# Optimization experiments

Hardware: AMD Instinct MI355X
Metric: run time of the kernel (lower is better)

The kernel has to match this reference:

```python
import jax, jax.numpy as jnp
import numpy as np

B, N = 16, 16          # batch, boxes per image
H, W = 640, 640        # image size
PH, PW = 300, 300      # learned patch size
MIN_AREA = 60.0
MAX_ANG = 20.0 * np.pi / 180.0


def setup_inputs() -> dict:
    key = jax.random.key(0)
    k1, k2, k3 = jax.random.split(key, 3)
    images = jax.random.uniform(k1, (B, H, W, 3), jnp.float32, -1.0, 1.0)
    patch = jax.random.uniform(k2, (PH, PW, 3), jnp.float32, -1.0, 1.0)
    kb1, kb2, kb3 = jax.random.split(k3, 3)
    ymin = jax.random.uniform(kb1, (B, N), jnp.float32, 0.0, H - 220.0)
    xmin = jax.random.uniform(kb2, (B, N), jnp.float32, 0.0, W - 220.0)
    hw = jax.random.uniform(kb3, (B, N, 2), jnp.float32, 100.0, 200.0)
    boxes = jnp.stack([ymin, xmin, ymin + hw[..., 0], xmin + hw[..., 1]], axis=-1)
    scale = jnp.float32(0.4)
    return {"boxes": boxes, "images": images, "patch": patch, "scale": scale}


def _bilinear(img, ys, xs):
    # img [Ph,Pw,3]; ys,xs [H,W] continuous source coords -> [H,W,3]
    Ph, Pw = img.shape[0], img.shape[1]
    y0 = jnp.floor(ys)
    x0 = jnp.floor(xs)
    wy = (ys - y0)[..., None]
    wx = (xs - x0)[..., None]
    y0i = jnp.clip(y0.astype(jnp.int32), 0, Ph - 1)
    y1i = jnp.clip(y0i + 1, 0, Ph - 1)
    x0i = jnp.clip(x0.astype(jnp.int32), 0, Pw - 1)
    x1i = jnp.clip(x0i + 1, 0, Pw - 1)
    v00 = img[y0i, x0i]
    v01 = img[y0i, x1i]
    v10 = img[y1i, x0i]
    v11 = img[y1i, x1i]
    return v00 * (1 - wy) * (1 - wx) + v01 * (1 - wy) * wx + v10 * wy * (1 - wx) + v11 * wy * wx


def _per_image(img, boxes_i, patch, scale, key):
    # random_print_adjust: per-channel affine jitter of the patch
    kw, kb, kloop = jax.random.split(key, 3)
    w = jax.random.normal(kw, (1, 1, 3), jnp.float32) * 0.1 + 0.5
    b = jax.random.normal(kb, (1, 1, 3), jnp.float32) * 0.01
    p = jnp.clip(w * patch + b, -1.0, 1.0)
    # BrightnessMatcher: shift patch mean brightness to match the image
    p = jnp.clip(p + (jnp.mean(img) - jnp.mean(p)), -1.0, 1.0)

    oimg = img
    mask0 = jnp.zeros_like(img)
    yy, xx = jnp.meshgrid(jnp.arange(H, dtype=jnp.float32),
                          jnp.arange(W, dtype=jnp.float32), indexing="ij")

    def step(carry, inp):
        image, mask = carry
        box, kk = inp
        ymin, xmin, ymax, xmax = box[0], box[1], box[2], box[3]
        h = ymax - ymin
        ww = xmax - xmin
        longer = jnp.maximum(h, ww)
        ps = jnp.floor(longer * scale)                       # patch_h == patch_w
        diag = jnp.minimum(jnp.sqrt(2.0).astype(jnp.float32) * ps, jnp.float32(W))
        oy = ymin + h / 2.0
        ox = xmin + ww / 2.0
        y0 = jnp.maximum(oy - diag / 2.0, 0.0)
        x0 = jnp.maximum(ox - diag / 2.0, 0.0)
        y0 = jnp.where(y0 + diag > H, H - diag, y0)
        x0 = jnp.where(x0 + diag > W, W - diag, x0)
        # int casts as in the TF code (values are >= 0, trunc == floor)
        y0i = jnp.floor(y0)
        x0i = jnp.floor(x0)
        phi = jnp.maximum(jnp.floor(ps), 1.0)
        diagi = jnp.floor(diag)
        valid_box = (phi * phi) > MIN_AREA

        k1, k2, k3 = jax.random.split(kk, 3)
        angle = jax.random.uniform(k1, (), jnp.float32, -MAX_ANG, MAX_ANG)

        # inverse warp: output pixel -> padded-patch coords -> resized-patch coords
        u = yy - y0i
        v = xx - x0i
        in_sq = (u >= 0) & (v >= 0) & (u < diagi) & (v < diagi)
        c = (diagi - 1.0) / 2.0
        ca, sa = jnp.cos(angle), jnp.sin(angle)
        su = c + ca * (u - c) - sa * (v - c)
        sv = c + sa * (u - c) + ca * (v - c)
        top = jnp.floor((diagi - phi) / 2.0)   # pad offset (floor top/left)
        py = su - top
        px = sv - top
        valid_src = (py >= 0) & (py <= phi - 1) & (px >= 0) & (px <= phi - 1)
        # resized-patch coords -> original patch coords (bilinear resize, half-pixel)
        sy = (py + 0.5) * (PH / phi) - 0.5
        sx = (px + 0.5) * (PW / phi) - 0.5
        samp = _bilinear(p, sy, sx)                                   # [H,W,3]
        noise = jax.random.uniform(k2, samp.shape, jnp.float32, -0.1, 0.1)
        bright = jax.random.uniform(k3, (), jnp.float32, -0.3, 0.3)
        im = jnp.clip(samp + noise + bright, -1.0, 1.0)
        val = jnp.where(valid_src[..., None], im, -2.0)
        val = jnp.where(val < -1.0, image, val)   # fill with current background
        val = jnp.clip(val, -1.0, 1.0)
        sel = (in_sq & valid_box)[..., None]
        new_image = jnp.where(sel, val, image)
        new_mask = jnp.where(sel, oimg - val, mask)
        return (new_image, new_mask), None

    keys = jax.random.split(kloop, N)
    (img_out, mask_out), _ = jax.lax.scan(step, (img, mask0), (boxes_i, keys))
    return img_out, mask_out


def reference(boxes, images, patch, scale):
    keys = jax.random.split(jax.random.key(42), B)
    img_out, mask_out = jax.vmap(_per_image, in_axes=(0, 0, None, None, 0))(
        images, boxes, patch, scale, keys)
    return img_out, mask_out
```

## Files before the change

### kernel.cpp

```cpp
#include <hip/hip_runtime.h>
#include <stdint.h>
#include <math.h>

#define B_ 16
#define N_ 16
#define H_ 640
#define W_ 640
#define PH_ 300
#define PW_ 300

#define IMG_ELEMS (H_*W_*3)
#define PATCH_ELEMS (PH_*PW_*3)

#define TROWS 16
#define TCOLS 64
#define TILES_Y (H_/TROWS)
#define TILES_X (W_/TCOLS)
#define TILES_PER_IMG (TILES_Y*TILES_X)
#define NTILES (B_*TILES_PER_IMG)
#define MAIN_GRID 2048

typedef float f32x4 __attribute__((ext_vector_type(4)));

__device__ __forceinline__ uint2 tf2x32(uint32_t k0, uint32_t k1, uint32_t x0, uint32_t x1) {
  uint32_t k2 = k0 ^ k1 ^ 0x1BD11BDAu;
#define TFR(r) x0 += x1; x1 = (x1 << (r)) | (x1 >> (32 - (r))); x1 ^= x0;
  x0 += k0; x1 += k1;
  TFR(13) TFR(15) TFR(26) TFR(6)
  x0 += k1; x1 += k2 + 1u;
  TFR(17) TFR(29) TFR(16) TFR(24)
  x0 += k2; x1 += k0 + 2u;
  TFR(13) TFR(15) TFR(26) TFR(6)
  x0 += k0; x1 += k1 + 3u;
  TFR(17) TFR(29) TFR(16) TFR(24)
  x0 += k1; x1 += k2 + 4u;
  TFR(13) TFR(15) TFR(26) TFR(6)
  x0 += k2; x1 += k0 + 5u;
#undef TFR
  return make_uint2(x0, x1);
}

__device__ __forceinline__ uint32_t rb32(uint32_t k0, uint32_t k1, uint32_t i) {
  uint2 o = tf2x32(k0, k1, 0u, i);
  return o.x ^ o.y;
}

__device__ __forceinline__ float u01f(uint32_t bits) {
  return __uint_as_float((bits >> 9) | 0x3F800000u) - 1.0f;
}

__device__ __forceinline__ float erfinv32(float x) {
  float w = -log1pf(-x * x);
  float p;
  if (w < 5.0f) {
    w = w - 2.5f;
    p = 2.81022636e-08f;
    p = fmaf(p, w, 3.43273939e-07f);
    p = fmaf(p, w, -3.5233877e-06f);
    p = fmaf(p, w, -4.39150654e-06f);
    p = fmaf(p, w, 0.00021858087f);
    p = fmaf(p, w, -0.00125372503f);
    p = fmaf(p, w, -0.00417768164f);
    p = fmaf(p, w, 0.246640727f);
    p = fmaf(p, w, 1.50140941f);
  } else {
    w = sqrtf(w) - 3.0f;
    p = -0.000200214257f;
    p = fmaf(p, w, 0.000100950558f);
    p = fmaf(p, w, 0.00134934322f);
    p = fmaf(p, w, -0.00367342844f);
    p = fmaf(p, w, 0.00573950773f);
    p = fmaf(p, w, -0.0076224613f);
    p = fmaf(p, w, 0.00943887047f);
    p = fmaf(p, w, 1.00167406f);
    p = fmaf(p, w, 2.83297682f);
  }
  return p * x;
}

__device__ __forceinline__ float jnormal(uint32_t bits) {
  float lo = __uint_as_float(0xBF7FFFFFu);
  float span = 1.0f - lo;
  float u = fmaxf(lo, u01f(bits) * span + lo);
  return 1.4142135623730951f * erfinv32(u);
}

__global__ __launch_bounds__(256) void reduce_kernel(
    const float* __restrict__ images, const float* __restrict__ patch,
    double* __restrict__ partials) {
  int b = blockIdx.y, j = blockIdx.x, t = threadIdx.x;
  __shared__ float swb[6];
  if (t < 6) {
    uint2 kb  = tf2x32(0u, 42u, 0u, (uint32_t)b);
    uint2 kw  = tf2x32(kb.x, kb.y, 0u, 0u);
    uint2 kbk = tf2x32(kb.x, kb.y, 0u, 1u);
    swb[t] = (t < 3) ? (jnormal(rb32(kw.x,  kw.y,  (uint32_t)t)) * 0.1f + 0.5f)
                     : (jnormal(rb32(kbk.x, kbk.y, (uint32_t)(t - 3))) * 0.01f);
  }
  __syncthreads();
  const float* img = images + (size_t)b * IMG_ELEMS;
  double s = 0.0;
  for (int i = j * 256 + t; i < IMG_ELEMS; i += 64 * 256) s += (double)img[i];
  float w0 = swb[0], w1 = swb[1], w2 = swb[2];
  float b0 = swb[3], b1 = swb[4], b2 = swb[5];
  double sp = 0.0;
  for (int i = j * 256 + t; i < PATCH_ELEMS; i += 64 * 256) {
    int q = i / 3; int ch = i - q * 3;
    float wv = (ch == 0) ? w0 : ((ch == 1) ? w1 : w2);
    float bv = (ch == 0) ? b0 : ((ch == 1) ? b1 : b2);
    float pv = fminf(fmaxf(wv * patch[i] + bv, -1.0f), 1.0f);
    sp += (double)pv;
  }
  __shared__ double sh[256];
  sh[t] = s; __syncthreads();
  for (int o = 128; o > 0; o >>= 1) { if (t < o) sh[t] += sh[t + o]; __syncthreads(); }
  if (t == 0) partials[((size_t)b * 64 + j) * 2 + 0] = sh[0];
  __syncthreads();
  sh[t] = sp; __syncthreads();
  for (int o = 128; o > 0; o >>= 1) { if (t < o) sh[t] += sh[t + o]; __syncthreads(); }
  if (t == 0) partials[((size_t)b * 64 + j) * 2 + 1] = sh[0];
}

__global__ void setup_finalize_kernel(
    const float* __restrict__ boxes, const float* __restrict__ scale_p,
    const double* __restrict__ partials,
    float* __restrict__ params, float* __restrict__ wb, float* __restrict__ dvals) {
  int t = threadIdx.x;
  if (t < B_) {
    double si = 0.0, sp = 0.0;
    for (int j = 0; j < 64; j++) {
      si += partials[((size_t)t * 64 + j) * 2 + 0];
      sp += partials[((size_t)t * 64 + j) * 2 + 1];
    }
    float mi = (float)(si / (double)IMG_ELEMS);
    float mp = (float)(sp / (double)PATCH_ELEMS);
    dvals[t] = mi - mp;
  }
  if (t >= B_*N_) return;
  int b = t >> 4, n = t & 15;
  uint2 kb = tf2x32(0u, 42u, 0u, (uint32_t)b);
  uint2 kw  = tf2x32(kb.x, kb.y, 0u, 0u);
  uint2 kbk = tf2x32(kb.x, kb.y, 0u, 1u);
  uint2 kl  = tf2x32(kb.x, kb.y, 0u, 2u);
  if (n == 0) {
    wb[b*8+0] = jnormal(rb32(kw.x,  kw.y,  0u)) * 0.1f + 0.5f;
    wb[b*8+1] = jnormal(rb32(kw.x,  kw.y,  1u)) * 0.1f + 0.5f;
    wb[b*8+2] = jnormal(rb32(kw.x,  kw.y,  2u)) * 0.1f + 0.5f;
    wb[b*8+3] = jnormal(rb32(kbk.x, kbk.y, 0u)) * 0.01f;
    wb[b*8+4] = jnormal(rb32(kbk.x, kbk.y, 1u)) * 0.01f;
    wb[b*8+5] = jnormal(rb32(kbk.x, kbk.y, 2u)) * 0.01f;
  }
  uint2 kk = tf2x32(kl.x, kl.y, 0u, (uint32_t)n);
  uint2 k1 = tf2x32(kk.x, kk.y, 0u, 0u);
  uint2 k2 = tf2x32(kk.x, kk.y, 0u, 1u);
  uint2 k3 = tf2x32(kk.x, kk.y, 0u, 2u);
  const float MA = (float)(20.0 * 3.14159265358979323846 / 180.0);
  float angle  = fmaxf(-MA,   u01f(rb32(k1.x, k1.y, 0u)) * (MA - (-MA)) + (-MA));
  float bright = fmaxf(-0.3f, u01f(rb32(k3.x, k3.y, 0u)) * (0.3f - (-0.3f)) + (-0.3f));

  const float* bx = boxes + (size_t)t * 4;
  float ymin = bx[0], xmin = bx[1], ymax = bx[2], xmax = bx[3];
  float sc = scale_p[0];
  float h = ymax - ymin, ww = xmax - xmin;
  float longer = fmaxf(h, ww);
  float ps = floorf(longer * sc);
  float diag = fminf(sqrtf(2.0f) * ps, (float)W_);
  float oy = ymin + h * 0.5f;
  float ox = xmin + ww * 0.5f;
  float y0 = fmaxf(oy - diag * 0.5f, 0.0f);
  float x0 = fmaxf(ox - diag * 0.5f, 0.0f);
  if (y0 + diag > (float)H_) y0 = (float)H_ - diag;
  if (x0 + diag > (float)W_) x0 = (float)W_ - diag;
  float y0i = floorf(y0), x0i = floorf(x0);
  float phi = fmaxf(floorf(ps), 1.0f);
  float diagi = floorf(diag);
  float validf = ((phi * phi) > 60.0f) ? 1.0f : 0.0f;
  float c = (diagi - 1.0f) * 0.5f;
  float top = floorf((diagi - phi) * 0.5f);

  float* P = params + t * 16;
  P[0] = y0i; P[1] = x0i; P[2] = diagi; P[3] = phi;
  P[4] = c;
  P[5] = (float)cos((double)angle);
  P[6] = (float)sin((double)angle);
  P[7] = top;
  P[8] = bright; P[9] = (float)PH_ / phi; P[10] = 0.0f; P[11] = validf;
  P[12] = __uint_as_float(k2.x); P[13] = __uint_as_float(k2.y); P[14] = 0.0f; P[15] = 0.0f;
}

__global__ __launch_bounds__(256) void main_kernel(
    const float* __restrict__ images, const float* __restrict__ patch,
    const float* __restrict__ params, const float* __restrict__ wb,
    const float* __restrict__ dvals, float* __restrict__ out) {
  __shared__ float sP[N_ * 16];
  __shared__ float sWB[6];
  __shared__ float sT[TROWS * 192];

  int bid = blockIdx.x;
  int b  = (bid & 7) * 2 + ((bid >> 3) & 1);
  int tid = threadIdx.x;

  if (tid < N_ * 16) sP[tid] = params[b * N_ * 16 + tid];
  if (tid < 6) sWB[tid] = wb[b * 8 + tid];
  __syncthreads();

  int lane = tid & 63;
  int wv   = tid >> 6;
  size_t ibase = (size_t)b * IMG_ELEMS;
  size_t moff  = (size_t)B_ * IMG_ELEMS;
  float dsh = dvals[b];

  int ck[3], lrk[3];
#pragma unroll
  for (int k = 0; k < 3; k++) {
    int t4 = k * 64 + lane;
    int r  = t4 / 48;
    ck[k]  = t4 - r * 48;
    lrk[k] = wv * 4 + r;
  }

  const float* Pc = sP + (tid & 15) * 16;
  float cP0 = Pc[0], cP1 = Pc[1], cLast = Pc[2] - 1.0f;
  bool cValid = (Pc[11] != 0.0f);

  for (int g = bid; g < NTILES; g += MAIN_GRID) {
    int tl = g >> 4;
    int ty = tl / TILES_X;
    int tx = tl - ty * TILES_X;

    float ys = (float)(ty * TROWS), ye = ys + (float)(TROWS - 1);
    float xs = (float)(tx * TCOLS), xe = xs + (float)(TCOLS - 1);
    bool hit = cValid && !(cP0 + cLast < ys || cP0 > ye)
                      && !(cP1 + cLast < xs || cP1 > xe);
    uint32_t mask = (uint32_t)(__ballot(hit) & 0xFFFFull);

    size_t fbk[3];
#pragma unroll
    for (int k = 0; k < 3; k++)
      fbk[k] = ibase + ((size_t)(ty * TROWS + lrk[k]) * W_ + tx * TCOLS) * 3 + (size_t)ck[k] * 4;

    if (mask == 0u) {
      const f32x4 z = {0.0f, 0.0f, 0.0f, 0.0f};
#pragma unroll
      for (int k = 0; k < 3; k++) {
        f32x4 d = *(const f32x4*)(images + fbk[k]);
        *(f32x4*)(out + fbk[k]) = d;
        *(f32x4*)(out + moff + fbk[k]) = z;
      }
      continue;
    }

#pragma unroll
    for (int k = 0; k < 3; k++) {
      f32x4 d = *(const f32x4*)(images + fbk[k]);
      *(f32x4*)(&sT[lrk[k] * 192 + ck[k] * 4]) = d;
    }

    int   pj[4];  float yfj[4];
    float xf = (float)(tx * TCOLS + lane);
#pragma unroll
    for (int j = 0; j < 4; j++) {
      int row = ty * TROWS + wv * 4 + j;
      pj[j]  = row * W_ + tx * TCOLS + lane;
      yfj[j] = (float)row;
    }

    float orig[12], img[12], mkv[12];
#pragma unroll
    for (int j = 0; j < 4; j++) {
      int base = (wv * 4 + j) * 192 + lane * 3;
      orig[j*3+0] = sT[base + 0];
      orig[j*3+1] = sT[base + 1];
      orig[j*3+2] = sT[base + 2];
    }
#pragma unroll
    for (int e = 0; e < 12; e++) { img[e] = orig[e]; mkv[e] = 0.0f; }

    uint32_t m = mask;
    while (m) {
      int n = __builtin_ctz(m);
      m &= m - 1u;
      const float* P = sP + n * 16;
      float P0 = P[0], P1 = P[1], diagi = P[2];
      float phi = P[3], c = P[4], ca = P[5], sa = P[6], top = P[7], bright = P[8], sph = P[9];
      uint32_t k2a = __float_as_uint(P[12]);
      uint32_t k2b = __float_as_uint(P[13]);
      float v = xf - P1;
      bool vok = (v >= 0.0f && v < diagi);
      float t2 = v - c;
#pragma unroll
      for (int j = 0; j < 4; j++) {
        float u = yfj[j] - P0;
        if (!(u >= 0.0f && u < diagi)) continue;
        if (!vok) continue;
        float t1 = u - c;
        float su = (c + ca * t1) - sa * t2;
        float sv = (c + sa * t1) + ca * t2;
        float py = su - top;
        float px = sv - top;
        bool vsrc = (py >= 0.0f) && (py <= phi - 1.0f) && (px >= 0.0f) && (px <= phi - 1.0f);
        if (vsrc) {
          float sy = (py + 0.5f) * sph - 0.5f;
          float sx = (px + 0.5f) * sph - 0.5f;
          float fy = floorf(sy), fx = floorf(sx);
          float wy = sy - fy, wxv = sx - fx;
          int iy0 = min(max((int)fy, 0), PH_ - 1);
          int iy1 = min(iy0 + 1, PH_ - 1);
          int ix0 = min(max((int)fx, 0), PW_ - 1);
          int ix1 = min(ix0 + 1, PW_ - 1);
          int o00 = (iy0 * PW_ + ix0) * 3;
          int o01 = (iy0 * PW_ + ix1) * 3;
          int o10 = (iy1 * PW_ + ix0) * 3;
          int o11 = (iy1 * PW_ + ix1) * 3;
          float omwy = 1.0f - wy, omwx = 1.0f - wxv;
          int nbase = pj[j] * 3;
#pragma unroll
          for (int ch = 0; ch < 3; ch++) {
            float wv2 = sWB[ch], bv = sWB[3 + ch];
            float a00 = fminf(fmaxf(wv2 * patch[o00 + ch] + bv, -1.0f), 1.0f);
            float a01 = fminf(fmaxf(wv2 * patch[o01 + ch] + bv, -1.0f), 1.0f);
            float a10 = fminf(fmaxf(wv2 * patch[o10 + ch] + bv, -1.0f), 1.0f);
            float a11 = fminf(fmaxf(wv2 * patch[o11 + ch] + bv, -1.0f), 1.0f);
            a00 = fminf(fmaxf(a00 + dsh, -1.0f), 1.0f);
            a01 = fminf(fmaxf(a01 + dsh, -1.0f), 1.0f);
            a10 = fminf(fmaxf(a10 + dsh, -1.0f), 1.0f);
            a11 = fminf(fmaxf(a11 + dsh, -1.0f), 1.0f);
            float samp = ((a00 * omwy) * omwx) + ((a01 * omwy) * wxv)
                       + ((a10 * wy) * omwx) + ((a11 * wy) * wxv);
            uint32_t bits = rb32(k2a, k2b, (uint32_t)(nbase + ch));
            float nz = fmaxf(-0.1f, u01f(bits) * (0.1f - (-0.1f)) + (-0.1f));
            float imv = fminf(fmaxf((samp + nz) + bright, -1.0f), 1.0f);
            img[j * 3 + ch] = imv;
            mkv[j * 3 + ch] = orig[j * 3 + ch] - imv;
          }
        } else {
#pragma unroll
          for (int ch = 0; ch < 3; ch++) mkv[j * 3 + ch] = orig[j * 3 + ch] - img[j * 3 + ch];
        }
      }
    }

#pragma unroll
    for (int j = 0; j < 4; j++) {
      int base = (wv * 4 + j) * 192 + lane * 3;
      sT[base + 0] = img[j*3+0];
      sT[base + 1] = img[j*3+1];
      sT[base + 2] = img[j*3+2];
    }
#pragma unroll
    for (int k = 0; k < 3; k++) {
      f32x4 d = *(const f32x4*)(&sT[lrk[k] * 192 + ck[k] * 4]);
      *(f32x4*)(out + fbk[k]) = d;
    }
#pragma unroll
    for (int j = 0; j < 4; j++) {
      int base = (wv * 4 + j) * 192 + lane * 3;
      sT[base + 0] = mkv[j*3+0];
      sT[base + 1] = mkv[j*3+1];
      sT[base + 2] = mkv[j*3+2];
    }
#pragma unroll
    for (int k = 0; k < 3; k++) {
      f32x4 d = *(const f32x4*)(&sT[lrk[k] * 192 + ck[k] * 4]);
      *(f32x4*)(out + moff + fbk[k]) = d;
    }
  }
}

extern "C" void kernel_launch(void* const* d_in, const int* in_sizes, int n_in,
                              void* d_out, int out_size, void* d_ws, size_t ws_size,
                              hipStream_t stream) {
  const float* boxes  = (const float*)d_in[0];
  const float* images = (const float*)d_in[1];
  const float* patch  = (const float*)d_in[2];
  const float* scale  = (const float*)d_in[3];
  float* out = (float*)d_out;

  float* params = (float*)d_ws;
  float* wb     = params + B_ * N_ * 16;
  float* dvals  = wb + B_ * 8;
  double* partials = (double*)((char*)d_ws + 20480);

  reduce_kernel<<<dim3(64, B_), 256, 0, stream>>>(images, patch, partials);
  setup_finalize_kernel<<<1, 256, 0, stream>>>(boxes, scale, partials, params, wb, dvals);
  main_kernel<<<MAIN_GRID, 256, 0, stream>>>(images, patch, params, wb, dvals, out);
}
```

Baseline: 291.3 us.

## Fuse reduce, setup and main kernels into one persistent kernel with grid barrier

Merges the mean-reduction, per-box parameter setup and main compositing kernels into a single persistent launch of 1024 blocks. Each block computes its own box parameters in shared memory and one slice of the reduction, then copies tiles no box touches while it waits on an atomic-counter grid barrier. After the barrier it reads all partial sums to get the brightness shift and composites the tiles that boxes hit. This removes two kernel launches and overlaps the reduction with the untouched-tile copy, but it adds a memset, a spin-wait barrier that deadlocks unless all 1024 blocks are resident at once, and a smaller grid.

New measurement: 434.6 us. +49.2%, slower.

```diff
diff --git a/kernel.cpp b/kernel.cpp
--- a/kernel.cpp
+++ b/kernel.cpp
@@ -18,7 +18,7 @@
 #define TILES_X (W_/TCOLS)
 #define TILES_PER_IMG (TILES_Y*TILES_X)
 #define NTILES (B_*TILES_PER_IMG)
-#define MAIN_GRID 2048
+#define GRID_N 1024
 
 typedef float f32x4 __attribute__((ext_vector_type(4)));
 
@@ -85,131 +85,111 @@
   return 1.4142135623730951f * erfinv32(u);
 }
 
-__global__ __launch_bounds__(256) void reduce_kernel(
+__global__ __launch_bounds__(256, 4) void fused_kernel(
+    const float* __restrict__ boxes, const float* __restrict__ scale_p,
     const float* __restrict__ images, const float* __restrict__ patch,
-    double* __restrict__ partials) {
-  int b = blockIdx.y, j = blockIdx.x, t = threadIdx.x;
-  __shared__ float swb[6];
-  if (t < 6) {
+    double* partials, unsigned int* cnt, float* __restrict__ out) {
+  __shared__ float sP[N_ * 16];
+  __shared__ float sWB[6];
+  __shared__ float swbR[6];
+  __shared__ float sD[1];
+  __shared__ double sh[256];
+  __shared__ float sT[TROWS * 192];
+
+  int bid = blockIdx.x;
+  int tid = threadIdx.x;
+  int b   = (bid & 7) * 2 + ((bid >> 3) & 1);
+  int jr  = bid & 63;
+  int br  = bid >> 6;
+
+  if (tid < N_) {
+    int n = tid;
+    int t = b * N_ + n;
+    uint2 kb = tf2x32(0u, 42u, 0u, (uint32_t)b);
+    uint2 kl = tf2x32(kb.x, kb.y, 0u, 2u);
+    uint2 kk = tf2x32(kl.x, kl.y, 0u, (uint32_t)n);
+    uint2 k1 = tf2x32(kk.x, kk.y, 0u, 0u);
+    uint2 k2 = tf2x32(kk.x, kk.y, 0u, 1u);
+    uint2 k3 = tf2x32(kk.x, kk.y, 0u, 2u);
+    const float MA = (float)(20.0 * 3.14159265358979323846 / 180.0);
+    float angle  = fmaxf(-MA,   u01f(rb32(k1.x, k1.y, 0u)) * (MA - (-MA)) + (-MA));
+    float bright = fmaxf(-0.3f, u01f(rb32(k3.x, k3.y, 0u)) * (0.3f - (-0.3f)) + (-0.3f));
+
+    const float* bx = boxes + (size_t)t * 4;
+    float ymin = bx[0], xmin = bx[1], ymax = bx[2], xmax = bx[3];
+    float sc = scale_p[0];
+    float h = ymax - ymin, ww = xmax - xmin;
+    float longer = fmaxf(h, ww);
+    float ps = floorf(longer * sc);
+    float diag = fminf(sqrtf(2.0f) * ps, (float)W_);
+    float oy = ymin + h * 0.5f;
+    float ox = xmin + ww * 0.5f;
+    float y0 = fmaxf(oy - diag * 0.5f, 0.0f);
+    float x0 = fmaxf(ox - diag * 0.5f, 0.0f);
+    if (y0 + diag > (float)H_) y0 = (float)H_ - diag;
+    if (x0 + diag > (float)W_) x0 = (float)W_ - diag;
+    float y0i = floorf(y0), x0i = floorf(x0);
+    float phi = fmaxf(floorf(ps), 1.0f);
+    float diagi = floorf(diag);
+    float validf = ((phi * phi) > 60.0f) ? 1.0f : 0.0f;
+    float c = (diagi - 1.0f) * 0.5f;
+    float top = floorf((diagi - phi) * 0.5f);
+
+    float* P = sP + n * 16;
+    P[0] = y0i; P[1] = x0i; P[2] = diagi; P[3] = phi;
+    P[4] = c;
+    P[5] = (float)cos((double)angle);
+    P[6] = (float)sin((double)angle);
+    P[7] = top;
+    P[8] = bright; P[9] = (float)PH_ / phi; P[10] = 0.0f; P[11] = validf;
+    P[12] = __uint_as_float(k2.x); P[13] = __uint_as_float(k2.y);
+    P[14] = 0.0f; P[15] = 0.0f;
+  }
+  if (tid < 6) {
     uint2 kb  = tf2x32(0u, 42u, 0u, (uint32_t)b);
     uint2 kw  = tf2x32(kb.x, kb.y, 0u, 0u);
     uint2 kbk = tf2x32(kb.x, kb.y, 0u, 1u);
-    swb[t] = (t < 3) ? (jnormal(rb32(kw.x,  kw.y,  (uint32_t)t)) * 0.1f + 0.5f)
-                     : (jnormal(rb32(kbk.x, kbk.y, (uint32_t)(t - 3))) * 0.01f);
+    sWB[tid] = (tid < 3) ? (jnormal(rb32(kw.x,  kw.y,  (uint32_t)tid)) * 0.1f + 0.5f)
+                         : (jnormal(rb32(kbk.x, kbk.y, (uint32_t)(tid - 3))) * 0.01f);
+    uint2 kbR  = tf2x32(0u, 42u, 0u, (uint32_t)br);
+    uint2 kwR  = tf2x32(kbR.x, kbR.y, 0u, 0u);
+    uint2 kbkR = tf2x32(kbR.x, kbR.y, 0u, 1u);
+    swbR[tid] = (tid < 3) ? (jnormal(rb32(kwR.x,  kwR.y,  (uint32_t)tid)) * 0.1f + 0.5f)
+                          : (jnormal(rb32(kbkR.x, kbkR.y, (uint32_t)(tid - 3))) * 0.01f);
   }
   __syncthreads();
-  const float* img = images + (size_t)b * IMG_ELEMS;
-  double s = 0.0;
-  for (int i = j * 256 + t; i < IMG_ELEMS; i += 64 * 256) s += (double)img[i];
-  float w0 = swb[0], w1 = swb[1], w2 = swb[2];
-  float b0 = swb[3], b1 = swb[4], b2 = swb[5];
-  double sp = 0.0;
-  for (int i = j * 256 + t; i < PATCH_ELEMS; i += 64 * 256) {
-    int q = i / 3; int ch = i - q * 3;
-    float wv = (ch == 0) ? w0 : ((ch == 1) ? w1 : w2);
-    float bv = (ch == 0) ? b0 : ((ch == 1) ? b1 : b2);
-    float pv = fminf(fmaxf(wv * patch[i] + bv, -1.0f), 1.0f);
-    sp += (double)pv;
-  }
-  __shared__ double sh[256];
-  sh[t] = s; __syncthreads();
-  for (int o = 128; o > 0; o >>= 1) { if (t < o) sh[t] += sh[t + o]; __syncthreads(); }
-  if (t == 0) partials[((size_t)b * 64 + j) * 2 + 0] = sh[0];
-  __syncthreads();
-  sh[t] = sp; __syncthreads();
-  for (int o = 128; o > 0; o >>= 1) { if (t < o) sh[t] += sh[t + o]; __syncthreads(); }
-  if (t == 0) partials[((size_t)b * 64 + j) * 2 + 1] = sh[0];
-}
-
-__global__ void setup_finalize_kernel(
-    const float* __restrict__ boxes, const float* __restrict__ scale_p,
-    const double* __restrict__ partials,
-    float* __restrict__ params, float* __restrict__ wb, float* __restrict__ dvals) {
-  int t = threadIdx.x;
-  if (t < B_) {
-    double si = 0.0, sp = 0.0;
-    for (int j = 0; j < 64; j++) {
-      si += partials[((size_t)t * 64 + j) * 2 + 0];
-      sp += partials[((size_t)t * 64 + j) * 2 + 1];
-    }
-    float mi = (float)(si / (double)IMG_ELEMS);
-    float mp = (float)(sp / (double)PATCH_ELEMS);
-    dvals[t] = mi - mp;
-  }
-  if (t >= B_*N_) return;
-  int b = t >> 4, n = t & 15;
-  uint2 kb = tf2x32(0u, 42u, 0u, (uint32_t)b);
-  uint2 kw  = tf2x32(kb.x, kb.y, 0u, 0u);
-  uint2 kbk = tf2x32(kb.x, kb.y, 0u, 1u);
-  uint2 kl  = tf2x32(kb.x, kb.y, 0u, 2u);
-  if (n == 0) {
-    wb[b*8+0] = jnormal(rb32(kw.x,  kw.y,  0u)) * 0.1f + 0.5f;
-    wb[b*8+1] = jnormal(rb32(kw.x,  kw.y,  1u)) * 0.1f + 0.5f;
-    wb[b*8+2] = jnormal(rb32(kw.x,  kw.y,  2u)) * 0.1f + 0.5f;
-    wb[b*8+3] = jnormal(rb32(kbk.x, kbk.y, 0u)) * 0.01f;
-    wb[b*8+4] = jnormal(rb32(kbk.x, kbk.y, 1u)) * 0.01f;
-    wb[b*8+5] = jnormal(rb32(kbk.x, kbk.y, 2u)) * 0.01f;
-  }
-  uint2 kk = tf2x32(kl.x, kl.y, 0u, (uint32_t)n);
-  uint2 k1 = tf2x32(kk.x, kk.y, 0u, 0u);
-  uint2 k2 = tf2x32(kk.x, kk.y, 0u, 1u);
-  uint2 k3 = tf2x32(kk.x, kk.y, 0u, 2u);
-  const float MA = (float)(20.0 * 3.14159265358979323846 / 180.0);
-  float angle  = fmaxf(-MA,   u01f(rb32(k1.x, k1.y, 0u)) * (MA - (-MA)) + (-MA));
-  float bright = fmaxf(-0.3f, u01f(rb32(k3.x, k3.y, 0u)) * (0.3f - (-0.3f)) + (-0.3f));
-
-  const float* bx = boxes + (size_t)t * 4;
-  float ymin = bx[0], xmin = bx[1], ymax = bx[2], xmax = bx[3];
-  float sc = scale_p[0];
-  float h = ymax - ymin, ww = xmax - xmin;
-  float longer = fmaxf(h, ww);
-  float ps = floorf(longer * sc);
-  float diag = fminf(sqrtf(2.0f) * ps, (float)W_);
-  float oy = ymin + h * 0.5f;
-  float ox = xmin + ww * 0.5f;
-  float y0 = fmaxf(oy - diag * 0.5f, 0.0f);
-  float x0 = fmaxf(ox - diag * 0.5f, 0.0f);
-  if (y0 + diag > (float)H_) y0 = (float)H_ - diag;
-  if (x0 + diag > (float)W_) x0 = (float)W_ - diag;
-  float y0i = floorf(y0), x0i = floorf(x0);
-  float phi = fmaxf(floorf(ps), 1.0f);
-  float diagi = floorf(diag);
-  float validf = ((phi * phi) > 60.0f) ? 1.0f : 0.0f;
-  float c = (diagi - 1.0f) * 0.5f;
-  float top = floorf((diagi - phi) * 0.5f);
-
-  float* P = params + t * 16;
-  P[0] = y0i; P[1] = x0i; P[2] = diagi; P[3] = phi;
-  P[4] = c;
-  P[5] = (float)cos((double)angle);
-  P[6] = (float)sin((double)angle);
-  P[7] = top;
-  P[8] = bright; P[9] = (float)PH_ / phi; P[10] = 0.0f; P[11] = validf;
-  P[12] = __uint_as_float(k2.x); P[13] = __uint_as_float(k2.y); P[14] = 0.0f; P[15] = 0.0f;
-}
-
-__global__ __launch_bounds__(256) void main_kernel(
-    const float* __restrict__ images, const float* __restrict__ patch,
-    const float* __restrict__ params, const float* __restrict__ wb,
-    const float* __restrict__ dvals, float* __restrict__ out) {
-  __shared__ float sP[N_ * 16];
-  __shared__ float sWB[6];
-  __shared__ float sT[TROWS * 192];
-
-  int bid = blockIdx.x;
-  int b  = (bid & 7) * 2 + ((bid >> 3) & 1);
-  int tid = threadIdx.x;
-
-  if (tid < N_ * 16) sP[tid] = params[b * N_ * 16 + tid];
-  if (tid < 6) sWB[tid] = wb[b * 8 + tid];
-  __syncthreads();
+
+  {
+    const float* img = images + (size_t)br * IMG_ELEMS;
+    double s = 0.0;
+    for (int i = jr * 256 + tid; i < IMG_ELEMS; i += 64 * 256) s += (double)img[i];
+    float w0 = swbR[0], w1 = swbR[1], w2 = swbR[2];
+    float b0 = swbR[3], b1 = swbR[4], b2 = swbR[5];
+    double sp = 0.0;
+    for (int i = jr * 256 + tid; i < PATCH_ELEMS; i += 64 * 256) {
+      int q = i / 3; int ch = i - q * 3;
+      float wv = (ch == 0) ? w0 : ((ch == 1) ? w1 : w2);
+      float bv = (ch == 0) ? b0 : ((ch == 1) ? b1 : b2);
+      float pv = fminf(fmaxf(wv * patch[i] + bv, -1.0f), 1.0f);
+      sp += (double)pv;
+    }
+    sh[tid] = s; __syncthreads();
+    for (int o = 128; o > 0; o >>= 1) { if (tid < o) sh[tid] += sh[tid + o]; __syncthreads(); }
+    if (tid == 0) partials[((size_t)br * 64 + jr) * 2 + 0] = sh[0];
+    __syncthreads();
+    sh[tid] = sp; __syncthreads();
+    for (int o = 128; o > 0; o >>= 1) { if (tid < o) sh[tid] += sh[tid + o]; __syncthreads(); }
+    if (tid == 0) {
+      partials[((size_t)br * 64 + jr) * 2 + 1] = sh[0];
+      __threadfence();
+      atomicAdd(cnt, 1u);
+    }
+  }
 
   int lane = tid & 63;
   int wv   = tid >> 6;
   size_t ibase = (size_t)b * IMG_ELEMS;
   size_t moff  = (size_t)B_ * IMG_ELEMS;
-  float dsh = dvals[b];
-
   int ck[3], lrk[3];
 #pragma unroll
   for (int k = 0; k < 3; k++) {
@@ -218,40 +198,65 @@
     ck[k]  = t4 - r * 48;
     lrk[k] = wv * 4 + r;
   }
-
   const float* Pc = sP + (tid & 15) * 16;
   float cP0 = Pc[0], cP1 = Pc[1], cLast = Pc[2] - 1.0f;
   bool cValid = (Pc[11] != 0.0f);
 
-  for (int g = bid; g < NTILES; g += MAIN_GRID) {
+  for (int g = bid; g < NTILES; g += GRID_N) {
     int tl = g >> 4;
     int ty = tl / TILES_X;
     int tx = tl - ty * TILES_X;
-
     float ys = (float)(ty * TROWS), ye = ys + (float)(TROWS - 1);
     float xs = (float)(tx * TCOLS), xe = xs + (float)(TCOLS - 1);
     bool hit = cValid && !(cP0 + cLast < ys || cP0 > ye)
                       && !(cP1 + cLast < xs || cP1 > xe);
     uint32_t mask = (uint32_t)(__ballot(hit) & 0xFFFFull);
+    if (mask != 0u) continue;
+    const f32x4 z = {0.0f, 0.0f, 0.0f, 0.0f};
+#pragma unroll
+    for (int k = 0; k < 3; k++) {
+      size_t fb = ibase + ((size_t)(ty * TROWS + lrk[k]) * W_ + tx * TCOLS) * 3 + (size_t)ck[k] * 4;
+      f32x4 d = *(const f32x4*)(images + fb);
+      *(f32x4*)(out + fb) = d;
+      *(f32x4*)(out + moff + fb) = z;
+    }
+  }
+
+  if (tid == 0) {
+    while (atomicAdd(cnt, 0u) < (unsigned int)GRID_N) __builtin_amdgcn_s_sleep(16);
+  }
+  __syncthreads();
+  __threadfence();
+
+  if (tid < 64) {
+    double pi_ = atomicAdd(&partials[((size_t)b * 64 + tid) * 2 + 0], 0.0);
+    double pp_ = atomicAdd(&partials[((size_t)b * 64 + tid) * 2 + 1], 0.0);
+    double si = 0.0, sp = 0.0;
+    for (int j = 0; j < 64; j++) { si += __shfl(pi_, j); sp += __shfl(pp_, j); }
+    if (tid == 0) {
+      float mi = (float)(si / (double)IMG_ELEMS);
+      float mp = (float)(sp / (double)PATCH_ELEMS);
+      sD[0] = mi - mp;
+    }
+  }
+  __syncthreads();
+  float dsh = sD[0];
+
+  for (int g = bid; g < NTILES; g += GRID_N) {
+    int tl = g >> 4;
+    int ty = tl / TILES_X;
+    int tx = tl - ty * TILES_X;
+    float ys = (float)(ty * TROWS), ye = ys + (float)(TROWS - 1);
+    float xs = (float)(tx * TCOLS), xe = xs + (float)(TCOLS - 1);
+    bool hit = cValid && !(cP0 + cLast < ys || cP0 > ye)
+                      && !(cP1 + cLast < xs || cP1 > xe);
+    uint32_t mask = (uint32_t)(__ballot(hit) & 0xFFFFull);
+    if (mask == 0u) continue;
 
     size_t fbk[3];
 #pragma unroll
-    for (int k = 0; k < 3; k++)
+    for (int k = 0; k < 3; k++) {
       fbk[k] = ibase + ((size_t)(ty * TROWS + lrk[k]) * W_ + tx * TCOLS) * 3 + (size_t)ck[k] * 4;
-
-    if (mask == 0u) {
-      const f32x4 z = {0.0f, 0.0f, 0.0f, 0.0f};
-#pragma unroll
-      for (int k = 0; k < 3; k++) {
-        f32x4 d = *(const f32x4*)(images + fbk[k]);
-        *(f32x4*)(out + fbk[k]) = d;
-        *(f32x4*)(out + moff + fbk[k]) = z;
-      }
-      continue;
-    }
-
-#pragma unroll
-    for (int k = 0; k < 3; k++) {
       f32x4 d = *(const f32x4*)(images + fbk[k]);
       *(f32x4*)(&sT[lrk[k] * 192 + ck[k] * 4]) = d;
     }
@@ -376,12 +381,9 @@
   const float* scale  = (const float*)d_in[3];
   float* out = (float*)d_out;
 
-  float* params = (float*)d_ws;
-  float* wb     = params + B_ * N_ * 16;
-  float* dvals  = wb + B_ * 8;
-  double* partials = (double*)((char*)d_ws + 20480);
-
-  reduce_kernel<<<dim3(64, B_), 256, 0, stream>>>(images, patch, partials);
-  setup_finalize_kernel<<<1, 256, 0, stream>>>(boxes, scale, partials, params, wb, dvals);
-  main_kernel<<<MAIN_GRID, 256, 0, stream>>>(images, patch, params, wb, dvals, out);
-}
+  unsigned int* cnt = (unsigned int*)((char*)d_ws + 16960);
+  double* partials  = (double*)((char*)d_ws + 20480);
+
+  hipMemsetAsync(cnt, 0, 64, stream);
+  fused_kernel<<<GRID_N, 256, 0, stream>>>(boxes, scale, images, patch, partials, cnt, out);
+}
```

## Split image copy and mask zeroing into separate streaming kernel before paint pass

Applied to the files above, without the earlier changes.

Moves the plain copy of images into the output and the zeroing of the mask into a dedicated grid-stride streaming kernel. The paint kernel now skips tiles with no box overlap and only processes tiles hit by a box. Overlapping tiles get written twice (once by the stream kernel, again by the paint kernel), and an extra kernel launch is added. In exchange the streaming pass gets simple, coalesced, branch-free bandwidth behaviour.

Result: slower. 321.6 us (+10.4%).

```diff
diff --git a/kernel.cpp b/kernel.cpp
--- a/kernel.cpp
+++ b/kernel.cpp
@@ -18,7 +18,8 @@
 #define TILES_X (W_/TCOLS)
 #define TILES_PER_IMG (TILES_Y*TILES_X)
 #define NTILES (B_*TILES_PER_IMG)
-#define MAIN_GRID 2048
+#define PAINT_GRID 2048
+#define STREAM_GRID 2048
 
 typedef float f32x4 __attribute__((ext_vector_type(4)));
 
@@ -188,7 +189,21 @@
   P[12] = __uint_as_float(k2.x); P[13] = __uint_as_float(k2.y); P[14] = 0.0f; P[15] = 0.0f;
 }
 
-__global__ __launch_bounds__(256) void main_kernel(
+__global__ __launch_bounds__(256) void stream_kernel(
+    const float* __restrict__ images, float* __restrict__ out) {
+  const size_t TOTAL4 = (size_t)B_ * IMG_ELEMS / 4;
+  const f32x4* src = (const f32x4*)images;
+  f32x4* dimg = (f32x4*)out;
+  f32x4* dmsk = dimg + TOTAL4;
+  const f32x4 z = {0.0f, 0.0f, 0.0f, 0.0f};
+  for (size_t i = (size_t)blockIdx.x * 256 + threadIdx.x; i < TOTAL4;
+       i += (size_t)STREAM_GRID * 256) {
+    dimg[i] = src[i];
+    dmsk[i] = z;
+  }
+}
+
+__global__ __launch_bounds__(256) void paint_kernel(
     const float* __restrict__ images, const float* __restrict__ patch,
     const float* __restrict__ params, const float* __restrict__ wb,
     const float* __restrict__ dvals, float* __restrict__ out) {
@@ -223,7 +238,7 @@
   float cP0 = Pc[0], cP1 = Pc[1], cLast = Pc[2] - 1.0f;
   bool cValid = (Pc[11] != 0.0f);
 
-  for (int g = bid; g < NTILES; g += MAIN_GRID) {
+  for (int g = bid; g < NTILES; g += PAINT_GRID) {
     int tl = g >> 4;
     int ty = tl / TILES_X;
     int tx = tl - ty * TILES_X;
@@ -233,25 +248,12 @@
     bool hit = cValid && !(cP0 + cLast < ys || cP0 > ye)
                       && !(cP1 + cLast < xs || cP1 > xe);
     uint32_t mask = (uint32_t)(__ballot(hit) & 0xFFFFull);
+    if (mask == 0u) continue;
 
     size_t fbk[3];
 #pragma unroll
-    for (int k = 0; k < 3; k++)
+    for (int k = 0; k < 3; k++) {
       fbk[k] = ibase + ((size_t)(ty * TROWS + lrk[k]) * W_ + tx * TCOLS) * 3 + (size_t)ck[k] * 4;
-
-    if (mask == 0u) {
-      const f32x4 z = {0.0f, 0.0f, 0.0f, 0.0f};
-#pragma unroll
-      for (int k = 0; k < 3; k++) {
-        f32x4 d = *(const f32x4*)(images + fbk[k]);
-        *(f32x4*)(out + fbk[k]) = d;
-        *(f32x4*)(out + moff + fbk[k]) = z;
-      }
-      continue;
-    }
-
-#pragma unroll
-    for (int k = 0; k < 3; k++) {
       f32x4 d = *(const f32x4*)(images + fbk[k]);
       *(f32x4*)(&sT[lrk[k] * 192 + ck[k] * 4]) = d;
     }
@@ -383,5 +385,6 @@
 
   reduce_kernel<<<dim3(64, B_), 256, 0, stream>>>(images, patch, partials);
   setup_finalize_kernel<<<1, 256, 0, stream>>>(boxes, scale, partials, params, wb, dvals);
-  main_kernel<<<MAIN_GRID, 256, 0, stream>>>(images, patch, params, wb, dvals, out);
-}
+  stream_kernel<<<STREAM_GRID, 256, 0, stream>>>(images, out);
+  paint_kernel<<<PAINT_GRID, 256, 0, stream>>>(images, patch, params, wb, dvals, out);
+}
```
